# Kernel tuning notes

Hardware: AMD Instinct MI355X
Metric: run time of the kernel (lower is better)

Reference implementation:

```python
import jax, jax.numpy as jnp
import numpy as np

N, E, G = 50000, 800000, 128          # nodes, edges, graphs
L, T, F = 4, 4, 20                    # conv layers, towers, per-tower width
D = T * F                             # 80 = hidden dim
EDGE_DIM = 16
AVG_DEG_LOG = float(np.log(17.0))     # avg_deg['log'] for avg in-degree ~16
EPS_STD = 1e-5
EPS_BN = 1e-5


def setup_inputs() -> dict:
    ks = iter(jax.random.split(jax.random.key(0), 32))
    rn = lambda *s: jax.random.normal(next(ks), s, jnp.float32) * 0.1
    return dict(
        x=jax.random.randint(next(ks), (N, 9), 0, 16),
        edge_index=jax.random.randint(next(ks), (2, E), 0, N),
        batch=jnp.sort(jax.random.randint(next(ks), (N,), 0, G)),
        edge_attr=rn(E, EDGE_DIM),
        atom_emb=rn(9, 16, D),
        edge_w=rn(L, EDGE_DIM, F), edge_b=jnp.zeros((L, F), jnp.float32),
        pre_w1=rn(L, T, 3 * F, F), pre_b1=jnp.zeros((L, T, F), jnp.float32),
        pre_w2=rn(L, T, F, F), pre_b2=jnp.zeros((L, T, F), jnp.float32),
        post_w1=rn(L, T, 13 * F, F), post_b1=jnp.zeros((L, T, F), jnp.float32),
        post_w2=rn(L, T, F, F), post_b2=jnp.zeros((L, T, F), jnp.float32),
        lin_w=rn(L, D, D), lin_b=jnp.zeros((L, D), jnp.float32),
        bn_g=jnp.ones((L, D), jnp.float32), bn_b=jnp.zeros((L, D), jnp.float32),
        mlp_w1=rn(D, 40), mlp_b1=jnp.zeros(40, jnp.float32),
        mlp_w2=rn(40, 20), mlp_b2=jnp.zeros(20, jnp.float32),
        mlp_w3=rn(20, 1), mlp_b3=jnp.zeros(1, jnp.float32),
    )


def _net(x, edge_index, batch, edge_attr, atom_emb, edge_w, edge_b, pre_w1,
         pre_b1, pre_w2, pre_b2, post_w1, post_b1, post_w2, post_b2, lin_w,
         lin_b, bn_g, bn_b, mlp_w1, mlp_b1, mlp_w2, mlp_b2, mlp_w3, mlp_b3):
    src, dst = edge_index[0], edge_index[1]
    # AtomEncoder: sum of 9 categorical embeddings -> [N, D]
    h = atom_emb[jnp.arange(9)[None, :], x].sum(1)
    deg_raw = jax.ops.segment_sum(jnp.ones((E,), jnp.float32), dst, N)
    deg = jnp.clip(deg_raw, 1.0)
    has_edge = (deg_raw > 0)[:, None, None]
    d3 = deg[:, None, None]
    logd = jnp.log(deg + 1.0)[:, None, None]
    for l in range(L):  # 4 PNAConv + BN + ReLU + residual (dropout off / eval)
        xt = h.reshape(N, T, F)
        ea = edge_attr @ edge_w[l] + edge_b[l]                      # [E, F]
        # message: concat(x_i, x_j, edge) -> per-tower pre MLP
        m = jnp.concatenate([xt[dst], xt[src],
                             jnp.broadcast_to(ea[:, None, :], (E, T, F))], -1)
        m = jax.nn.relu(jnp.einsum('eti,tio->eto', m, pre_w1[l]) + pre_b1[l])
        m = jnp.einsum('eti,tio->eto', m, pre_w2[l]) + pre_b2[l]    # [E,T,F]
        # multi-aggregator scatter-reduce
        mean = jax.ops.segment_sum(m, dst, N) / d3
        msq = jax.ops.segment_sum(m * m, dst, N) / d3
        std = jnp.sqrt(jax.nn.relu(msq - mean * mean) + EPS_STD)
        mn = jnp.where(has_edge, jax.ops.segment_min(m, dst, N), 0.0)
        mx = jnp.where(has_edge, jax.ops.segment_max(m, dst, N), 0.0)
        agg = jnp.concatenate([mean, mn, mx, std], -1)              # [N,T,4F]
        # degree scalers: identity, amplification, attenuation
        out = jnp.concatenate([agg, agg * (logd / AVG_DEG_LOG),
                               agg * (AVG_DEG_LOG / logd)], -1)     # [N,T,12F]
        out = jnp.concatenate([xt, out], -1)                        # [N,T,13F]
        out = jax.nn.relu(jnp.einsum('nti,tio->nto', out, post_w1[l]) + post_b1[l])
        out = jnp.einsum('nti,tio->nto', out, post_w2[l]) + post_b2[l]
        out = out.reshape(N, D) @ lin_w[l] + lin_b[l]
        # BatchNorm over nodes (batch statistics)
        mu = out.mean(0)
        var = jnp.mean((out - mu) ** 2, axis=0)
        out = (out - mu) * (bn_g[l] / jnp.sqrt(var + EPS_BN)) + bn_b[l]
        h = jax.nn.relu(out) + h
    # global mean pool over graphs + readout MLP
    cnt = jnp.clip(jax.ops.segment_sum(jnp.ones((N,), jnp.float32), batch, G), 1.0)
    g = jax.ops.segment_sum(h, batch, G) / cnt[:, None]
    g = jax.nn.relu(g @ mlp_w1 + mlp_b1)
    g = jax.nn.relu(g @ mlp_w2 + mlp_b2)
    return g @ mlp_w3 + mlp_b3                                      # [G, 1]


def reference(x, edge_index, batch, edge_attr, atom_emb, edge_w, edge_b, pre_w1,
              pre_b1, pre_w2, pre_b2, post_w1, post_b1, post_w2, post_b2, lin_w,
              lin_b, bn_g, bn_b, mlp_w1, mlp_b1, mlp_w2, mlp_b2, mlp_w3, mlp_b3):
    return _net(x, edge_index, batch, edge_attr, atom_emb, edge_w, edge_b, pre_w1,
                pre_b1, pre_w2, pre_b2, post_w1, post_b1, post_w2, post_b2,
                lin_w, lin_b, bn_g, bn_b, mlp_w1, mlp_b1, mlp_w2, mlp_b2,
                mlp_w3, mlp_b3)
```

## Files before the change

### kernel.cpp

```cpp
#include <hip/hip_runtime.h>
#include <hip/hip_bf16.h>

#define NN 50000
#define EE 800000
#define GG 128
#define LL 4
#define TT 4
#define FF 20
#define DD 80
#define SCAN_B ((NN + 1023) / 1024)
#define TILE_N 16
#define ITEMS (TILE_N * 10)
static constexpr float AVG_LOG = 2.8332133440562162f;

typedef __fp16 half2v __attribute__((ext_vector_type(2)));

__device__ __forceinline__ float bf2f(unsigned short u) {
  return __uint_as_float((unsigned)u << 16);
}
__device__ __forceinline__ unsigned short f2bf(float f) {
  __hip_bfloat16 b = __float2bfloat16(f);
  return *(unsigned short*)&b;
}
__device__ __forceinline__ half2v pkrtz(float a, float b) {
#if __has_builtin(__builtin_amdgcn_cvt_pkrtz)
  return __builtin_amdgcn_cvt_pkrtz(a, b);
#else
  half2v h; h.x = (__fp16)a; h.y = (__fp16)b; return h;
#endif
}
__device__ __forceinline__ float fdot2(half2v a, half2v b, float c) {
#if __has_builtin(__builtin_amdgcn_fdot2)
  return __builtin_amdgcn_fdot2(a, b, c, false);
#else
  return fmaf((float)a.x, (float)b.x, fmaf((float)a.y, (float)b.y, c));
#endif
}
__device__ __forceinline__ half2v u2h2(unsigned int u) {
  return __builtin_bit_cast(half2v, u);
}
__device__ __forceinline__ unsigned int h22u(half2v h) {
  return __builtin_bit_cast(unsigned int, h);
}
__device__ __forceinline__ unsigned int packh2_rne(float a, float b) {
  half2v h; h.x = (__fp16)a; h.y = (__fp16)b;
  return h22u(h);
}
__device__ __forceinline__ unsigned int pack_bf16(float a, float b) {
  return (unsigned int)f2bf(a) | ((unsigned int)f2bf(b) << 16);
}

__global__ __launch_bounds__(256) void k_h(const int* __restrict__ x,
                                           const float* __restrict__ atom_emb,
                                           float* __restrict__ h) {
  int idx = blockIdx.x * 256 + threadIdx.x;
  if (idx >= NN * DD) return;
  int n = idx / DD, d = idx - n * DD;
  const int* xr = x + n * 9;
  float acc = 0.f;
#pragma unroll
  for (int i = 0; i < 9; ++i) {
    int v = xr[i];
    acc += atom_emb[(i * 16 + v) * DD + d];
  }
  h[idx] = acc;
}

__global__ __launch_bounds__(256) void k_deg(const int* __restrict__ ei, int* __restrict__ cnt) {
  int e = blockIdx.x * 256 + threadIdx.x;
  if (e >= EE) return;
  atomicAdd(&cnt[ei[EE + e]], 1);
}

__global__ __launch_bounds__(1024) void k_scan_sum(const int* __restrict__ cnt, int* __restrict__ bsum) {
  __shared__ int red[1024];
  int tid = threadIdx.x;
  int i = blockIdx.x * 1024 + tid;
  red[tid] = (i < NN) ? cnt[i] : 0;
  __syncthreads();
  for (int off = 512; off > 0; off >>= 1) {
    if (tid < off) red[tid] += red[tid + off];
    __syncthreads();
  }
  if (tid == 0) bsum[blockIdx.x] = red[0];
}

__global__ void k_scan_top(const int* __restrict__ bsum, int* __restrict__ boff,
                           int* __restrict__ row_ptr) {
  if (threadIdx.x == 0 && blockIdx.x == 0) {
    int acc = 0;
    for (int b = 0; b < SCAN_B; ++b) { boff[b] = acc; acc += bsum[b]; }
    row_ptr[NN] = acc;
  }
}

__global__ __launch_bounds__(1024) void k_scan_apply(const int* __restrict__ cnt,
                                                     const int* __restrict__ boff,
                                                     int* __restrict__ row_ptr,
                                                     int* __restrict__ cursor) {
  __shared__ int sm[1024];
  int tid = threadIdx.x;
  int i = blockIdx.x * 1024 + tid;
  int v = (i < NN) ? cnt[i] : 0;
  sm[tid] = v;
  __syncthreads();
  for (int off = 1; off < 1024; off <<= 1) {
    int t = (tid >= off) ? sm[tid - off] : 0;
    __syncthreads();
    sm[tid] += t;
    __syncthreads();
  }
  int excl = boff[blockIdx.x] + sm[tid] - v;
  if (i < NN) { row_ptr[i] = excl; cursor[i] = excl; }
}

__global__ __launch_bounds__(256) void k_csrfill(const int* __restrict__ ei,
                                                 int* __restrict__ cursor,
                                                 int* __restrict__ csr_src,
                                                 int* __restrict__ csr_eid,
                                                 int* __restrict__ csr_dst) {
  int e = blockIdx.x * 256 + threadIdx.x;
  if (e >= EE) return;
  int dst = ei[EE + e];
  int slot = atomicAdd(&cursor[dst], 1);
  csr_src[slot] = ei[e];
  csr_eid[slot] = e;
  csr_dst[slot] = dst;
}

__global__ __launch_bounds__(256) void k_eagather(const int* __restrict__ csr_eid,
                                                  const float* __restrict__ edge_attr,
                                                  unsigned int* __restrict__ ea16) {
  int sl = blockIdx.x * 256 + threadIdx.x;
  if (sl >= EE) return;
  int e = csr_eid[sl];
  const float4* ap = (const float4*)(edge_attr + (size_t)e * 16);
  uint4 o0, o1;
  float4 v0 = ap[0], v1 = ap[1], v2 = ap[2], v3 = ap[3];
  o0.x = packh2_rne(v0.x, v0.y); o0.y = packh2_rne(v0.z, v0.w);
  o0.z = packh2_rne(v1.x, v1.y); o0.w = packh2_rne(v1.z, v1.w);
  o1.x = packh2_rne(v2.x, v2.y); o1.y = packh2_rne(v2.z, v2.w);
  o1.z = packh2_rne(v3.x, v3.y); o1.w = packh2_rne(v3.z, v3.w);
  uint4* op = (uint4*)(ea16 + (size_t)sl * 8);
  op[0] = o0; op[1] = o1;
}

__global__ __launch_bounds__(256) void k_nodeparams(const int* __restrict__ cnt,
                                                    float* __restrict__ inv_deg,
                                                    float* __restrict__ s1a,
                                                    float* __restrict__ s2a) {
  int n = blockIdx.x * 256 + threadIdx.x;
  if (n >= NN) return;
  int c = cnt[n];
  float deg = (c > 0) ? (float)c : 1.0f;
  inv_deg[n] = 1.0f / deg;
  float logd = logf(deg + 1.0f);
  s1a[n] = logd / AVG_LOG;
  s2a[n] = AVG_LOG / logd;
}

__global__ __launch_bounds__(64) void k_wcomb(const float* __restrict__ edge_w,
                                              const float* __restrict__ edge_b,
                                              const float* __restrict__ pre_w1,
                                              const float* __restrict__ pre_b1,
                                              const float* __restrict__ pre_w2,
                                              const float* __restrict__ post_w1,
                                              const float* __restrict__ post_w2,
                                              unsigned int* __restrict__ wcpk,
                                              unsigned int* __restrict__ w2pk,
                                              unsigned int* __restrict__ q1pk,
                                              unsigned int* __restrict__ q2pk,
                                              float* __restrict__ biasc,
                                              float* __restrict__ colsum, int l) {
  int t = blockIdx.x;
  int wt = l * TT + t;
  int j = threadIdx.x;
  if (t == 0) {
    for (int i = threadIdx.x; i < 2 * DD; i += 64) colsum[i] = 0.f;
  }
  if (j >= FF) return;
  const float* W1 = pre_w1 + (size_t)wt * 1200;
  const float* W2 = pre_w2 + (size_t)wt * 400;
  const float* ew = edge_w + (size_t)l * 16 * FF;
  const float* eb = edge_b + (size_t)l * FF;
  float col[16];
  for (int i = 0; i < 16; ++i) {
    float acc = 0.f;
#pragma unroll
    for (int f = 0; f < FF; ++f) acc = fmaf(ew[i * FF + f], W1[(40 + f) * FF + j], acc);
    col[i] = acc;
  }
#pragma unroll
  for (int i2 = 0; i2 < 8; ++i2)
    wcpk[((size_t)t * FF + j) * 8 + i2] = packh2_rne(col[2 * i2], col[2 * i2 + 1]);
#pragma unroll
  for (int i2 = 0; i2 < 10; ++i2)
    w2pk[((size_t)t * FF + j) * 10 + i2] = packh2_rne(W2[(2 * i2) * FF + j], W2[(2 * i2 + 1) * FF + j]);
  float b = pre_b1[wt * FF + j];
#pragma unroll
  for (int f = 0; f < FF; ++f) b = fmaf(eb[f], W1[(40 + f) * FF + j], b);
  biasc[t * FF + j] = b;
  const float* Q1 = post_w1 + (size_t)wt * 5200;
  const float* Q2 = post_w2 + (size_t)wt * 400;
  for (int i2 = 0; i2 < 120; ++i2) {
    int blk = i2 / 40, k = i2 - blk * 40;
    int r0 = 20 + 80 * blk + 2 * k;
    q1pk[((size_t)t * 120 + i2) * FF + j] = packh2_rne(Q1[r0 * FF + j], Q1[(r0 + 1) * FF + j]);
  }
#pragma unroll
  for (int i2 = 0; i2 < 10; ++i2)
    q2pk[((size_t)t * 10 + i2) * FF + j] = packh2_rne(Q2[(2 * i2) * FF + j], Q2[(2 * i2 + 1) * FF + j]);
}

__global__ __launch_bounds__(256) void k_prenode(
    const float* __restrict__ h, const float* __restrict__ pre_w1,
    const float* __restrict__ biasc,
    unsigned short* __restrict__ predD, unsigned short* __restrict__ predS, int l) {
  int tid = threadIdx.x;
  int t = tid >> 6, lane = tid & 63;
  int n = blockIdx.x * 64 + lane;
  if (n >= NN) return;
  int wt_u = __builtin_amdgcn_readfirstlane(l * TT + t);
  const float* W1 = pre_w1 + (size_t)wt_u * 1200;
  const float* bc = biasc + t * FF;
  float xt[FF];
  {
    const float4* pp = (const float4*)(h + (size_t)n * DD + t * FF);
#pragma unroll
    for (int i = 0; i < 5; ++i) { float4 v = pp[i]; xt[i*4]=v.x; xt[i*4+1]=v.y; xt[i*4+2]=v.z; xt[i*4+3]=v.w; }
  }
  float d[FF], s[FF];
#pragma unroll
  for (int j = 0; j < FF; ++j) { d[j] = bc[j]; s[j] = 0.f; }
#pragma unroll
  for (int i = 0; i < FF; ++i) {
    float a = xt[i];
#pragma unroll
    for (int j = 0; j < FF; ++j) {
      d[j] = fmaf(a, W1[i * FF + j], d[j]);
      s[j] = fmaf(a, W1[(FF + i) * FF + j], s[j]);
    }
  }
  ushort4* pd = (ushort4*)(predD + (size_t)n * DD + t * FF);
  ushort4* ps = (ushort4*)(predS + (size_t)n * DD + t * FF);
#pragma unroll
  for (int i = 0; i < 5; ++i) {
    pd[i] = make_ushort4(f2bf(d[i*4]), f2bf(d[i*4+1]), f2bf(d[i*4+2]), f2bf(d[i*4+3]));
    ps[i] = make_ushort4(f2bf(s[i*4]), f2bf(s[i*4+1]), f2bf(s[i*4+2]), f2bf(s[i*4+3]));
  }
}

__global__ __launch_bounds__(256, 4) void k_preagg(
    const unsigned short* __restrict__ predD,
    const unsigned short* __restrict__ predS,
    const unsigned int* __restrict__ ea16,
    const int* __restrict__ csr_src,
    const int* __restrict__ csr_dst,
    const int* __restrict__ row_ptr,
    const float* __restrict__ inv_deg,
    const unsigned int* __restrict__ wcpk,
    const unsigned int* __restrict__ w2pk,
    const float* __restrict__ pre_b2,
    unsigned short* __restrict__ aggbuf,
    int l) {
  __shared__ int nbr[TILE_N + 1];
  __shared__ float dDs[TT][TILE_N * FF];
  __shared__ unsigned int m2w[TT][128 * 11];
  int tid = threadIdx.x;
  int t = tid >> 6, lane = tid & 63;
  int t_u = __builtin_amdgcn_readfirstlane(t);
  int n0 = blockIdx.x * TILE_N;
  const unsigned int* Wcp = wcpk + (size_t)t_u * FF * 8;
  const unsigned int* W2p = w2pk + (size_t)t_u * FF * 10;
  const float* b2 = pre_b2 + (size_t)(l * TT + t_u) * FF;

  if (tid <= TILE_N) {
    int node = n0 + tid; if (node > NN) node = NN;
    nbr[tid] = row_ptr[node];
  }
  for (int i = lane; i < TILE_N * FF; i += 64) {
    int ni = i / FF, ch = i - ni * FF;
    int node = n0 + ni;
    dDs[t][i] = (node < NN) ? bf2f(predD[(size_t)node * DD + t_u * FF + ch]) : 0.f;
  }
  __syncthreads();
  int tbeg = nbr[0], tend = nbr[TILE_N];

  int itN[3], itP[3], itB[3], itE[3];
#pragma unroll
  for (int k = 0; k < 3; ++k) {
    int it = lane + 64 * k;
    bool v = it < ITEMS;
    int nd = v ? (it / 10) : 0;
    itN[k] = nd;
    itP[k] = v ? (it - nd * 10) : 0;
    itB[k] = v ? nbr[nd] : 0;
    itE[k] = v ? nbr[nd + 1] : 0;
  }
  float sS[3][2], sQ[3][2], sN[3][2], sX[3][2];
#pragma unroll
  for (int k = 0; k < 3; ++k) {
    sS[k][0] = 0.f; sS[k][1] = 0.f; sQ[k][0] = 0.f; sQ[k][1] = 0.f;
    sN[k][0] = 3.4e38f; sN[k][1] = 3.4e38f; sX[k][0] = -3.4e38f; sX[k][1] = -3.4e38f;
  }

  for (int wb = tbeg; wb < tend; wb += 128) {
#pragma unroll
    for (int e = 0; e < 2; ++e) {
      int sl = lane + 64 * e;
      int p = wb + sl;
      if (p < tend) {
        int src = csr_src[p];
        int ni = csr_dst[p] - n0;
        float m1[FF];
        {
          const float4* dd = (const float4*)(&dDs[t][ni * FF]);
          const ushort4* qq = (const ushort4*)(predS + (size_t)src * DD + t_u * FF);
#pragma unroll
          for (int i = 0; i < 5; ++i) {
            float4 d4 = dd[i];
            ushort4 v = qq[i];
            m1[i*4+0] = d4.x + bf2f(v.x);
            m1[i*4+1] = d4.y + bf2f(v.y);
            m1[i*4+2] = d4.z + bf2f(v.z);
            m1[i*4+3] = d4.w + bf2f(v.w);
          }
        }
        half2v eap[8];
        {
          const uint4* ep = (const uint4*)(ea16 + (size_t)p * 8);
          uint4 e0 = ep[0], e1 = ep[1];
          eap[0] = u2h2(e0.x); eap[1] = u2h2(e0.y); eap[2] = u2h2(e0.z); eap[3] = u2h2(e0.w);
          eap[4] = u2h2(e1.x); eap[5] = u2h2(e1.y); eap[6] = u2h2(e1.z); eap[7] = u2h2(e1.w);
        }
#pragma unroll
        for (int j = 0; j < FF; ++j) {
          float c = m1[j];
#pragma unroll
          for (int i2 = 0; i2 < 8; ++i2) c = fdot2(eap[i2], u2h2(Wcp[j * 8 + i2]), c);
          m1[j] = c;
        }
        half2v mp[10];
#pragma unroll
        for (int pr = 0; pr < 10; ++pr)
          mp[pr] = pkrtz(fmaxf(m1[2*pr], 0.f), fmaxf(m1[2*pr+1], 0.f));
        float m2[FF];
#pragma unroll
        for (int j = 0; j < FF; ++j) {
          float c = b2[j];
#pragma unroll
          for (int i2 = 0; i2 < 10; ++i2) c = fdot2(mp[i2], u2h2(W2p[j * 10 + i2]), c);
          m2[j] = c;
        }
        unsigned int* row = &m2w[t][sl * 11];
#pragma unroll
        for (int pr = 0; pr < 10; ++pr) row[pr] = h22u(pkrtz(m2[2*pr], m2[2*pr+1]));
      }
    }
    __syncthreads();
    int we = (wb + 128 < tend) ? (wb + 128) : tend;
#pragma unroll
    for (int k = 0; k < 3; ++k) {
      int lo = itB[k] > wb ? itB[k] : wb;
      int hi = itE[k] < we ? itE[k] : we;
      for (int s = lo; s < hi; ++s) {
        half2v h2 = u2h2(m2w[t][(s - wb) * 11 + itP[k]]);
        float v0 = (float)h2.x, v1 = (float)h2.y;
        sS[k][0] += v0; sQ[k][0] = fmaf(v0, v0, sQ[k][0]);
        sN[k][0] = fminf(sN[k][0], v0); sX[k][0] = fmaxf(sX[k][0], v0);
        sS[k][1] += v1; sQ[k][1] = fmaf(v1, v1, sQ[k][1]);
        sN[k][1] = fminf(sN[k][1], v1); sX[k][1] = fmaxf(sX[k][1], v1);
      }
    }
    __syncthreads();
  }

#pragma unroll
  for (int k = 0; k < 3; ++k) {
    int it = lane + 64 * k;
    if (it < ITEMS) {
      int n = n0 + itN[k];
      if (n < NN) {
        float inv = inv_deg[n];
        bool noe = (itE[k] <= itB[k]);
        float mu0 = sS[k][0] * inv, mu1 = sS[k][1] * inv;
        float sd0 = sqrtf(fmaxf(sQ[k][0] * inv - mu0 * mu0, 0.f) + 1e-5f);
        float sd1 = sqrtf(fmaxf(sQ[k][1] * inv - mu1 * mu1, 0.f) + 1e-5f);
        float mn0 = noe ? 0.f : sN[k][0], mn1 = noe ? 0.f : sN[k][1];
        float mx0 = noe ? 0.f : sX[k][0], mx1 = noe ? 0.f : sX[k][1];
        unsigned short* ab = aggbuf + ((size_t)n * 4 + t_u) * 80;
        ((unsigned int*)(ab))[itP[k]]      = pack_bf16(mu0, mu1);
        ((unsigned int*)(ab + 20))[itP[k]] = pack_bf16(mn0, mn1);
        ((unsigned int*)(ab + 40))[itP[k]] = pack_bf16(mx0, mx1);
        ((unsigned int*)(ab + 60))[itP[k]] = pack_bf16(sd0, sd1);
      }
    }
  }
}

__global__ __launch_bounds__(256) void k_postlin(
    const float* __restrict__ h, const unsigned short* __restrict__ aggbuf,
    const float* __restrict__ s1a, const float* __restrict__ s2a,
    const float* __restrict__ post_w1, const float* __restrict__ post_b1,
    const unsigned int* __restrict__ q1pk, const unsigned int* __restrict__ q2pk,
    const float* __restrict__ post_b2,
    const float* __restrict__ lin_w, const float* __restrict__ lin_b,
    float* __restrict__ outl, float* __restrict__ colsum, int l) {
  __shared__ float rows[5280];
  __shared__ unsigned int lq1[TT * 120 * FF];
  __shared__ unsigned int lq2[TT * 10 * FF];
  int tid = threadIdx.x;
  int t = tid >> 6, lane = tid & 63;
  int t_u = __builtin_amdgcn_readfirstlane(t);
  int wt_u = __builtin_amdgcn_readfirstlane(l * TT + t);
  int n = blockIdx.x * 64 + lane;
  bool nvalid = (n < NN);

  float xt[FF];
  uint4 araw[10];
  {
    const float4* pp = (const float4*)(h + (size_t)(nvalid ? n : 0) * DD + t_u * FF);
#pragma unroll
    for (int i = 0; i < 5; ++i) { float4 v = pp[i]; xt[i*4]=v.x; xt[i*4+1]=v.y; xt[i*4+2]=v.z; xt[i*4+3]=v.w; }
    const uint4* ap = (const uint4*)(aggbuf + ((size_t)(nvalid ? n : 0) * 4 + t_u) * 80);
#pragma unroll
    for (int q = 0; q < 10; ++q) araw[q] = ap[q];
  }
  float c1 = s1a[nvalid ? n : 0], c2 = s2a[nvalid ? n : 0];

  {
    const uint4* s1p = (const uint4*)q1pk;
    uint4* d1 = (uint4*)lq1;
    for (int i = tid; i < TT * 120 * FF / 4; i += 256) d1[i] = s1p[i];
    const uint4* s2p = (const uint4*)q2pk;
    uint4* d2 = (uint4*)lq2;
    for (int i = tid; i < TT * 10 * FF / 4; i += 256) d2[i] = s2p[i];
  }
  __syncthreads();

  const float* Q1 = post_w1 + (size_t)wt_u * 5200;
  const float* B1 = post_b1 + (size_t)wt_u * FF;
  const float* B2 = post_b2 + (size_t)wt_u * FF;
  const unsigned int* q1 = lq1 + t_u * 120 * FF;
  const unsigned int* q2 = lq2 + t_u * 10 * FF;
  if (nvalid) {
    half2v c1p = pkrtz(c1, c1), c2p = pkrtz(c2, c2);
    half2v a0p[40];
#pragma unroll
    for (int q = 0; q < 10; ++q) {
      unsigned int w[4] = {araw[q].x, araw[q].y, araw[q].z, araw[q].w};
#pragma unroll
      for (int k = 0; k < 4; ++k) {
        unsigned int u = w[k];
        float lo = __uint_as_float(u << 16);
        float hi = __uint_as_float(u & 0xffff0000u);
        a0p[q * 4 + k] = pkrtz(lo, hi);
      }
    }
    float o1[FF];
#pragma unroll
    for (int j = 0; j < FF; ++j) o1[j] = B1[j];
#pragma unroll
    for (int i = 0; i < FF; ++i) {
      float a = xt[i];
#pragma unroll
      for (int j = 0; j < FF; ++j) o1[j] = fmaf(a, Q1[i * FF + j], o1[j]);
    }
#pragma unroll 2
    for (int k = 0; k < 40; ++k) {
      half2v act = a0p[k];
      const unsigned int* wr = q1 + k * FF;
#pragma unroll
      for (int j = 0; j < FF; ++j) o1[j] = fdot2(act, u2h2(wr[j]), o1[j]);
    }
#pragma unroll 2
    for (int k = 0; k < 40; ++k) {
      half2v act = a0p[k] * c1p;
      const unsigned int* wr = q1 + (40 + k) * FF;
#pragma unroll
      for (int j = 0; j < FF; ++j) o1[j] = fdot2(act, u2h2(wr[j]), o1[j]);
    }
#pragma unroll 2
    for (int k = 0; k < 40; ++k) {
      half2v act = a0p[k] * c2p;
      const unsigned int* wr = q1 + (80 + k) * FF;
#pragma unroll
      for (int j = 0; j < FF; ++j) o1[j] = fdot2(act, u2h2(wr[j]), o1[j]);
    }
    half2v o1p[10];
#pragma unroll
    for (int i2 = 0; i2 < 10; ++i2)
      o1p[i2] = pkrtz(fmaxf(o1[2*i2], 0.f), fmaxf(o1[2*i2+1], 0.f));
    float o2[FF];
#pragma unroll
    for (int j = 0; j < FF; ++j) o2[j] = B2[j];
#pragma unroll 2
    for (int i2 = 0; i2 < 10; ++i2) {
      half2v act = o1p[i2];
      const unsigned int* wr = q2 + i2 * FF;
#pragma unroll
      for (int j = 0; j < FF; ++j) o2[j] = fdot2(act, u2h2(wr[j]), o2[j]);
    }
#pragma unroll
    for (int j = 0; j < FF; ++j) rows[lane * 81 + t_u * FF + j] = o2[j];
  } else {
#pragma unroll
    for (int j = 0; j < FF; ++j) rows[lane * 81 + t_u * FF + j] = 0.f;
  }
  __syncthreads();

  int n2 = blockIdx.x * 64 + lane;
  const float* WlG = lin_w + (size_t)l * DD * DD + t_u * FF;
  float acc[FF];
#pragma unroll
  for (int j = 0; j < FF; ++j) acc[j] = lin_b[l * DD + t_u * FF + j];
  for (int i = 0; i < DD; ++i) {
    float r = rows[lane * 81 + i];
    const float* wl = WlG + i * DD;
#pragma unroll
    for (int j = 0; j < FF; ++j) acc[j] = fmaf(r, wl[j], acc[j]);
  }
  bool valid = (n2 < NN);
  __syncthreads();

#pragma unroll
  for (int j = 0; j < FF; ++j) rows[(t_u * FF + j) * 66 + lane] = valid ? acc[j] : 0.f;
  __syncthreads();
  if (tid < DD) {
    float s = 0.f;
    for (int k = 0; k < 64; ++k) s += rows[tid * 66 + k];
    atomicAdd(&colsum[tid], s);
  }
  {
    int nb = blockIdx.x * 64;
    for (int i = tid; i < 64 * 20; i += 256) {
      int nl = i / 20;
      int c4 = (i - nl * 20) * 4;
      int gn = nb + nl;
      if (gn < NN) {
        float4 v = make_float4(rows[(c4 + 0) * 66 + nl], rows[(c4 + 1) * 66 + nl],
                               rows[(c4 + 2) * 66 + nl], rows[(c4 + 3) * 66 + nl]);
        *(float4*)(outl + (size_t)gn * DD + c4) = v;
      }
    }
  }
  __syncthreads();
#pragma unroll
  for (int j = 0; j < FF; ++j) rows[(t_u * FF + j) * 66 + lane] = valid ? acc[j] * acc[j] : 0.f;
  __syncthreads();
  if (tid < DD) {
    float s = 0.f;
    for (int k = 0; k < 64; ++k) s += rows[tid * 66 + k];
    atomicAdd(&colsum[DD + tid], s);
  }
}

__global__ __launch_bounds__(256) void k_bnapply(const float* __restrict__ outl,
                                                 const float* __restrict__ colsum,
                                                 const float* __restrict__ bn_g,
                                                 const float* __restrict__ bn_b,
                                                 float* __restrict__ h, int l) {
  __shared__ float sc[DD], ofs[DD];
  int tid = threadIdx.x;
  if (tid < DD) {
    float mu = colsum[tid] * (1.0f / NN);
    float var = colsum[DD + tid] * (1.0f / NN) - mu * mu;
    float s = bn_g[l * DD + tid] * rsqrtf(var + 1e-5f);
    sc[tid] = s;
    ofs[tid] = bn_b[l * DD + tid] - mu * s;
  }
  __syncthreads();
  int idx = blockIdx.x * 256 + tid;
  if (idx >= NN * DD) return;
  int d = idx % DD;
  float v = fmaf(outl[idx], sc[d], ofs[d]);
  h[idx] += fmaxf(v, 0.f);
}

__global__ __launch_bounds__(256) void k_gcnt(const int* __restrict__ batch, int* __restrict__ gcnt) {
  __shared__ int hcnt[GG];
  int tid = threadIdx.x;
  if (tid < GG) hcnt[tid] = 0;
  __syncthreads();
  int n = blockIdx.x * 256 + tid;
  if (n < NN) atomicAdd(&hcnt[batch[n]], 1);
  __syncthreads();
  if (tid < GG && hcnt[tid] > 0) atomicAdd(&gcnt[tid], hcnt[tid]);
}

__global__ void k_gstart(const int* __restrict__ gcnt, int* __restrict__ gstart) {
  if (threadIdx.x == 0 && blockIdx.x == 0) {
    int acc = 0;
    for (int g = 0; g < GG; ++g) { gstart[g] = acc; acc += gcnt[g]; }
  }
}

__global__ __launch_bounds__(320) void k_gmean(const float* __restrict__ h,
                                               const int* __restrict__ gstart,
                                               const int* __restrict__ gcnt,
                                               float* __restrict__ gbuf) {
  __shared__ float red[320];
  int g = blockIdx.x, tid = threadIdx.x;
  int nl = tid / DD, d = tid - nl * DD;
  int start = gstart[g], c = gcnt[g];
  float acc = 0.f;
  for (int r = start + nl; r < start + c; r += 4) acc += h[(size_t)r * DD + d];
  red[tid] = acc;
  __syncthreads();
  if (tid < DD) {
    float s = red[tid] + red[tid + DD] + red[tid + 2 * DD] + red[tid + 3 * DD];
    float cf = (c > 0) ? (float)c : 1.0f;
    gbuf[g * DD + tid] = s / cf;
  }
}

__global__ __launch_bounds__(64) void k_mlp(const float* __restrict__ gbuf,
                                            const float* __restrict__ w1, const float* __restrict__ b1,
                                            const float* __restrict__ w2, const float* __restrict__ b2,
                                            const float* __restrict__ w3, const float* __restrict__ b3,
                                            float* __restrict__ out) {
  __shared__ float row[DD];
  __shared__ float t1[40];
  __shared__ float t2[20];
  int g = blockIdx.x, tid = threadIdx.x;
  for (int i = tid; i < DD; i += 64) row[i] = gbuf[g * DD + i];
  __syncthreads();
  if (tid < 40) {
    float acc = b1[tid];
#pragma unroll
    for (int i = 0; i < DD; ++i) acc = fmaf(row[i], w1[i * 40 + tid], acc);
    t1[tid] = fmaxf(acc, 0.f);
  }
  __syncthreads();
  if (tid < 20) {
    float acc = b2[tid];
#pragma unroll
    for (int i = 0; i < 40; ++i) acc = fmaf(t1[i], w2[i * 20 + tid], acc);
    t2[tid] = fmaxf(acc, 0.f);
  }
  __syncthreads();
  if (tid == 0) {
    float acc = b3[0];
#pragma unroll
    for (int i = 0; i < 20; ++i) acc = fmaf(t2[i], w3[i], acc);
    out[g] = acc;
  }
}

extern "C" void kernel_launch(void* const* d_in, const int* in_sizes, int n_in,
                              void* d_out, int out_size, void* d_ws, size_t ws_size,
                              hipStream_t stream) {
  const int*   x         = (const int*)d_in[0];
  const int*   ei        = (const int*)d_in[1];
  const int*   batch     = (const int*)d_in[2];
  const float* edge_attr = (const float*)d_in[3];
  const float* atom_emb  = (const float*)d_in[4];
  const float* edge_w    = (const float*)d_in[5];
  const float* edge_b    = (const float*)d_in[6];
  const float* pre_w1    = (const float*)d_in[7];
  const float* pre_b1    = (const float*)d_in[8];
  const float* pre_w2    = (const float*)d_in[9];
  const float* pre_b2    = (const float*)d_in[10];
  const float* post_w1   = (const float*)d_in[11];
  const float* post_b1   = (const float*)d_in[12];
  const float* post_w2   = (const float*)d_in[13];
  const float* post_b2   = (const float*)d_in[14];
  const float* lin_w     = (const float*)d_in[15];
  const float* lin_b     = (const float*)d_in[16];
  const float* bn_g      = (const float*)d_in[17];
  const float* bn_b      = (const float*)d_in[18];
  const float* mlp_w1    = (const float*)d_in[19];
  const float* mlp_b1    = (const float*)d_in[20];
  const float* mlp_w2    = (const float*)d_in[21];
  const float* mlp_b2    = (const float*)d_in[22];
  const float* mlp_w3    = (const float*)d_in[23];
  const float* mlp_b3    = (const float*)d_in[24];
  float* out = (float*)d_out;

  char* ws = (char*)d_ws;
  size_t off = 0;
  auto alloc = [&](size_t bytes) -> void* {
    void* p = ws + off;
    off += (bytes + 15) & ~(size_t)15;
    return p;
  };
  float* h       = (float*)alloc((size_t)NN * DD * 4);
  float* outl    = (float*)alloc((size_t)NN * DD * 4);
  unsigned short* predD = (unsigned short*)alloc((size_t)NN * DD * 2);
  unsigned short* predS = (unsigned short*)alloc((size_t)NN * DD * 2);
  int*   csr_src = (int*)alloc((size_t)EE * 4);
  int*   csr_eid = (int*)alloc((size_t)EE * 4);
  int*   csr_dst = (int*)alloc((size_t)EE * 4);
  unsigned int* ea16 = (unsigned int*)alloc((size_t)EE * 8 * 4);
  int*   row_ptr = (int*)alloc((size_t)(NN + 1) * 4);
  int*   cnt     = (int*)alloc((size_t)NN * 4);
  int*   cursor  = (int*)alloc((size_t)NN * 4);
  float* inv_deg = (float*)alloc((size_t)NN * 4);
  float* s1a     = (float*)alloc((size_t)NN * 4);
  float* s2a     = (float*)alloc((size_t)NN * 4);
  float* colsum  = (float*)alloc(2 * DD * 4);
  float* gbuf    = (float*)alloc((size_t)GG * DD * 4);
  unsigned int* wcpk  = (unsigned int*)alloc((size_t)TT * FF * 8 * 4);
  unsigned int* w2pk  = (unsigned int*)alloc((size_t)TT * FF * 10 * 4);
  unsigned int* q1pk  = (unsigned int*)alloc((size_t)TT * 120 * FF * 4);
  unsigned int* q2pk  = (unsigned int*)alloc((size_t)TT * 10 * FF * 4);
  float* biasc   = (float*)alloc((size_t)TT * FF * 4);
  int*   bsum    = (int*)alloc((size_t)SCAN_B * 4);
  int*   boff    = (int*)alloc((size_t)SCAN_B * 4);
  int*   gcnt    = (int*)alloc((size_t)GG * 4);
  int*   gstart  = (int*)alloc((size_t)(GG + 1) * 4);
  unsigned short* aggbuf = (unsigned short*)alloc((size_t)NN * 4 * 80 * 2);
  (void)in_sizes; (void)n_in; (void)out_size; (void)ws_size;

  hipMemsetAsync(cnt, 0, (size_t)NN * 4, stream);
  k_h<<<(NN * DD + 255) / 256, 256, 0, stream>>>(x, atom_emb, h);
  k_deg<<<(EE + 255) / 256, 256, 0, stream>>>(ei, cnt);
  k_scan_sum<<<SCAN_B, 1024, 0, stream>>>(cnt, bsum);
  k_scan_top<<<1, 64, 0, stream>>>(bsum, boff, row_ptr);
  k_scan_apply<<<SCAN_B, 1024, 0, stream>>>(cnt, boff, row_ptr, cursor);
  k_csrfill<<<(EE + 255) / 256, 256, 0, stream>>>(ei, cursor, csr_src, csr_eid, csr_dst);
  k_eagather<<<(EE + 255) / 256, 256, 0, stream>>>(csr_eid, edge_attr, ea16);
  k_nodeparams<<<(NN + 255) / 256, 256, 0, stream>>>(cnt, inv_deg, s1a, s2a);

  int tilesA = (NN + TILE_N - 1) / TILE_N;
  int blocksPL = (NN + 63) / 64;
  for (int l = 0; l < LL; ++l) {
    k_wcomb<<<TT, 64, 0, stream>>>(edge_w, edge_b, pre_w1, pre_b1, pre_w2,
        post_w1, post_w2, wcpk, w2pk, q1pk, q2pk, biasc, colsum, l);
    k_prenode<<<(NN + 63) / 64, 256, 0, stream>>>(h, pre_w1, biasc, predD, predS, l);
    k_preagg<<<tilesA, 256, 0, stream>>>(predD, predS, ea16, csr_src, csr_dst, row_ptr,
        inv_deg, wcpk, w2pk, pre_b2, aggbuf, l);
    k_postlin<<<blocksPL, 256, 0, stream>>>(h, aggbuf, s1a, s2a,
        post_w1, post_b1, q1pk, q2pk, post_b2, lin_w, lin_b, outl, colsum, l);
    k_bnapply<<<(NN * DD + 255) / 256, 256, 0, stream>>>(outl, colsum, bn_g, bn_b, h, l);
  }

  hipMemsetAsync(gcnt, 0, (size_t)GG * 4, stream);
  k_gcnt<<<(NN + 255) / 256, 256, 0, stream>>>(batch, gcnt);
  k_gstart<<<1, 64, 0, stream>>>(gcnt, gstart);
  k_gmean<<<GG, 320, 0, stream>>>(h, gstart, gcnt, gbuf);
  k_mlp<<<GG, 64, 0, stream>>>(gbuf, mlp_w1, mlp_b1, mlp_w2, mlp_b2, mlp_w3, mlp_b3, out);
}
```

Baseline: 1.358 ms.

## Fuse BatchNorm apply into next layer's pre-node kernel and shrink postlin LDS

For layers after the first, the BatchNorm, ReLU and residual update is folded into a new k_bnpre kernel. It recomputes h from outl and the previous layer's column sums, writes h back and immediately computes the pre-node projections. This removes one full read-write pass over h per layer and one launch. The column-sum buffers are double-buffered so that zeroing in k_wcomb does not clobber the statistics still needed. Separately, k_postlin now stages its intermediate rows as packed fp16 in a shared union buffer to reduce LDS use, at some precision cost.

```diff
diff --git a/kernel.cpp b/kernel.cpp
--- a/kernel.cpp
+++ b/kernel.cpp
@@ -171,12 +171,12 @@
                                               unsigned int* __restrict__ q1pk,
                                               unsigned int* __restrict__ q2pk,
                                               float* __restrict__ biasc,
-                                              float* __restrict__ colsum, int l) {
+                                              float* __restrict__ colsum_cur, int l) {
   int t = blockIdx.x;
   int wt = l * TT + t;
   int j = threadIdx.x;
   if (t == 0) {
-    for (int i = threadIdx.x; i < 2 * DD; i += 64) colsum[i] = 0.f;
+    for (int i = threadIdx.x; i < 2 * DD; i += 64) colsum_cur[i] = 0.f;
   }
   if (j >= FF) return;
   const float* W1 = pre_w1 + (size_t)wt * 1200;
@@ -243,6 +243,72 @@
   }
   ushort4* pd = (ushort4*)(predD + (size_t)n * DD + t * FF);
   ushort4* ps = (ushort4*)(predS + (size_t)n * DD + t * FF);
+#pragma unroll
+  for (int i = 0; i < 5; ++i) {
+    pd[i] = make_ushort4(f2bf(d[i*4]), f2bf(d[i*4+1]), f2bf(d[i*4+2]), f2bf(d[i*4+3]));
+    ps[i] = make_ushort4(f2bf(s[i*4]), f2bf(s[i*4+1]), f2bf(s[i*4+2]), f2bf(s[i*4+3]));
+  }
+}
+
+__global__ __launch_bounds__(256) void k_bnpre(
+    const float* __restrict__ outl, const float* __restrict__ colsum_prev,
+    const float* __restrict__ bn_g, const float* __restrict__ bn_b,
+    float* __restrict__ h,
+    const float* __restrict__ pre_w1, const float* __restrict__ biasc,
+    unsigned short* __restrict__ predD, unsigned short* __restrict__ predS,
+    int lprev, int l) {
+  __shared__ float sc[DD], ofs[DD];
+  int tid = threadIdx.x;
+  int t = tid >> 6, lane = tid & 63;
+  if (tid < DD) {
+    float mu = colsum_prev[tid] * (1.0f / NN);
+    float var = colsum_prev[DD + tid] * (1.0f / NN) - mu * mu;
+    float s = bn_g[lprev * DD + tid] * rsqrtf(var + 1e-5f);
+    sc[tid] = s;
+    ofs[tid] = bn_b[lprev * DD + tid] - mu * s;
+  }
+  __syncthreads();
+  int n = blockIdx.x * 64 + lane;
+  if (n >= NN) return;
+  int wt_u = __builtin_amdgcn_readfirstlane(l * TT + t);
+  int t_u = __builtin_amdgcn_readfirstlane(t);
+  const float* W1 = pre_w1 + (size_t)wt_u * 1200;
+  const float* bc = biasc + t_u * FF;
+  float xt[FF];
+  {
+    const float4* po = (const float4*)(outl + (size_t)n * DD + t_u * FF);
+    const float4* ph = (const float4*)(h + (size_t)n * DD + t_u * FF);
+#pragma unroll
+    for (int i = 0; i < 5; ++i) {
+      float4 vo = po[i];
+      float4 vh = ph[i];
+      int d0 = t_u * FF + i * 4;
+      xt[i*4+0] = vh.x + fmaxf(fmaf(vo.x, sc[d0+0], ofs[d0+0]), 0.f);
+      xt[i*4+1] = vh.y + fmaxf(fmaf(vo.y, sc[d0+1], ofs[d0+1]), 0.f);
+      xt[i*4+2] = vh.z + fmaxf(fmaf(vo.z, sc[d0+2], ofs[d0+2]), 0.f);
+      xt[i*4+3] = vh.w + fmaxf(fmaf(vo.w, sc[d0+3], ofs[d0+3]), 0.f);
+    }
+  }
+  {
+    float4* ph = (float4*)(h + (size_t)n * DD + t_u * FF);
+#pragma unroll
+    for (int i = 0; i < 5; ++i)
+      ph[i] = make_float4(xt[i*4], xt[i*4+1], xt[i*4+2], xt[i*4+3]);
+  }
+  float d[FF], s[FF];
+#pragma unroll
+  for (int j = 0; j < FF; ++j) { d[j] = bc[j]; s[j] = 0.f; }
+#pragma unroll
+  for (int i = 0; i < FF; ++i) {
+    float a = xt[i];
+#pragma unroll
+    for (int j = 0; j < FF; ++j) {
+      d[j] = fmaf(a, W1[i * FF + j], d[j]);
+      s[j] = fmaf(a, W1[(FF + i) * FF + j], s[j]);
+    }
+  }
+  ushort4* pd = (ushort4*)(predD + (size_t)n * DD + t_u * FF);
+  ushort4* ps = (ushort4*)(predS + (size_t)n * DD + t_u * FF);
 #pragma unroll
   for (int i = 0; i < 5; ++i) {
     pd[i] = make_ushort4(f2bf(d[i*4]), f2bf(d[i*4+1]), f2bf(d[i*4+2]), f2bf(d[i*4+3]));
@@ -406,9 +472,11 @@
     const float* __restrict__ post_b2,
     const float* __restrict__ lin_w, const float* __restrict__ lin_b,
     float* __restrict__ outl, float* __restrict__ colsum, int l) {
-  __shared__ float rows[5280];
-  __shared__ unsigned int lq1[TT * 120 * FF];
-  __shared__ unsigned int lq2[TT * 10 * FF];
+  __shared__ unsigned int smem[13024];
+  unsigned int* rowsU = smem;
+  unsigned int* lq1 = smem + 2624;
+  unsigned int* lq2 = smem + 2624 + 9600;
+  float* tbuf = (float*)(smem + 2624);
   int tid = threadIdx.x;
   int t = tid >> 6, lane = tid & 63;
   int t_u = __builtin_amdgcn_readfirstlane(t);
@@ -502,10 +570,11 @@
       for (int j = 0; j < FF; ++j) o2[j] = fdot2(act, u2h2(wr[j]), o2[j]);
     }
 #pragma unroll
-    for (int j = 0; j < FF; ++j) rows[lane * 81 + t_u * FF + j] = o2[j];
+    for (int pr = 0; pr < 10; ++pr)
+      rowsU[lane * 41 + t_u * 10 + pr] = packh2_rne(o2[2*pr], o2[2*pr+1]);
   } else {
 #pragma unroll
-    for (int j = 0; j < FF; ++j) rows[lane * 81 + t_u * FF + j] = 0.f;
+    for (int pr = 0; pr < 10; ++pr) rowsU[lane * 41 + t_u * 10 + pr] = 0;
   }
   __syncthreads();
 
@@ -514,21 +583,26 @@
   float acc[FF];
 #pragma unroll
   for (int j = 0; j < FF; ++j) acc[j] = lin_b[l * DD + t_u * FF + j];
-  for (int i = 0; i < DD; ++i) {
-    float r = rows[lane * 81 + i];
-    const float* wl = WlG + i * DD;
-#pragma unroll
-    for (int j = 0; j < FF; ++j) acc[j] = fmaf(r, wl[j], acc[j]);
+  for (int i2 = 0; i2 < 40; ++i2) {
+    half2v rp = u2h2(rowsU[lane * 41 + i2]);
+    float r0 = (float)rp.x, r1 = (float)rp.y;
+    const float* wl0 = WlG + (2 * i2) * DD;
+    const float* wl1 = WlG + (2 * i2 + 1) * DD;
+#pragma unroll
+    for (int j = 0; j < FF; ++j) {
+      acc[j] = fmaf(r0, wl0[j], acc[j]);
+      acc[j] = fmaf(r1, wl1[j], acc[j]);
+    }
   }
   bool valid = (n2 < NN);
   __syncthreads();
 
 #pragma unroll
-  for (int j = 0; j < FF; ++j) rows[(t_u * FF + j) * 66 + lane] = valid ? acc[j] : 0.f;
+  for (int j = 0; j < FF; ++j) tbuf[(t_u * FF + j) * 66 + lane] = valid ? acc[j] : 0.f;
   __syncthreads();
   if (tid < DD) {
     float s = 0.f;
-    for (int k = 0; k < 64; ++k) s += rows[tid * 66 + k];
+    for (int k = 0; k < 64; ++k) s += tbuf[tid * 66 + k];
     atomicAdd(&colsum[tid], s);
   }
   {
@@ -538,19 +612,19 @@
       int c4 = (i - nl * 20) * 4;
       int gn = nb + nl;
       if (gn < NN) {
-        float4 v = make_float4(rows[(c4 + 0) * 66 + nl], rows[(c4 + 1) * 66 + nl],
-                               rows[(c4 + 2) * 66 + nl], rows[(c4 + 3) * 66 + nl]);
+        float4 v = make_float4(tbuf[(c4 + 0) * 66 + nl], tbuf[(c4 + 1) * 66 + nl],
+                               tbuf[(c4 + 2) * 66 + nl], tbuf[(c4 + 3) * 66 + nl]);
         *(float4*)(outl + (size_t)gn * DD + c4) = v;
       }
     }
   }
   __syncthreads();
 #pragma unroll
-  for (int j = 0; j < FF; ++j) rows[(t_u * FF + j) * 66 + lane] = valid ? acc[j] * acc[j] : 0.f;
+  for (int j = 0; j < FF; ++j) tbuf[(t_u * FF + j) * 66 + lane] = valid ? acc[j] * acc[j] : 0.f;
   __syncthreads();
   if (tid < DD) {
     float s = 0.f;
-    for (int k = 0; k < 64; ++k) s += rows[tid * 66 + k];
+    for (int k = 0; k < 64; ++k) s += tbuf[tid * 66 + k];
     atomicAdd(&colsum[DD + tid], s);
   }
 }
@@ -698,7 +772,8 @@
   float* inv_deg = (float*)alloc((size_t)NN * 4);
   float* s1a     = (float*)alloc((size_t)NN * 4);
   float* s2a     = (float*)alloc((size_t)NN * 4);
-  float* colsum  = (float*)alloc(2 * DD * 4);
+  float* colsumA = (float*)alloc(2 * DD * 4);
+  float* colsumB = (float*)alloc(2 * DD * 4);
   float* gbuf    = (float*)alloc((size_t)GG * DD * 4);
   unsigned int* wcpk  = (unsigned int*)alloc((size_t)TT * FF * 8 * 4);
   unsigned int* w2pk  = (unsigned int*)alloc((size_t)TT * FF * 10 * 4);
@@ -712,6 +787,8 @@
   unsigned short* aggbuf = (unsigned short*)alloc((size_t)NN * 4 * 80 * 2);
   (void)in_sizes; (void)n_in; (void)out_size; (void)ws_size;
 
+  float* cs[2] = {colsumA, colsumB};
+
   hipMemsetAsync(cnt, 0, (size_t)NN * 4, stream);
   k_h<<<(NN * DD + 255) / 256, 256, 0, stream>>>(x, atom_emb, h);
   k_deg<<<(EE + 255) / 256, 256, 0, stream>>>(ei, cnt);
@@ -726,14 +803,19 @@
   int blocksPL = (NN + 63) / 64;
   for (int l = 0; l < LL; ++l) {
     k_wcomb<<<TT, 64, 0, stream>>>(edge_w, edge_b, pre_w1, pre_b1, pre_w2,
-        post_w1, post_w2, wcpk, w2pk, q1pk, q2pk, biasc, colsum, l);
-    k_prenode<<<(NN + 63) / 64, 256, 0, stream>>>(h, pre_w1, biasc, predD, predS, l);
+        post_w1, post_w2, wcpk, w2pk, q1pk, q2pk, biasc, cs[l & 1], l);
+    if (l == 0) {
+      k_prenode<<<blocksPL, 256, 0, stream>>>(h, pre_w1, biasc, predD, predS, l);
+    } else {
+      k_bnpre<<<blocksPL, 256, 0, stream>>>(outl, cs[(l - 1) & 1], bn_g, bn_b, h,
+          pre_w1, biasc, predD, predS, l - 1, l);
+    }
     k_preagg<<<tilesA, 256, 0, stream>>>(predD, predS, ea16, csr_src, csr_dst, row_ptr,
         inv_deg, wcpk, w2pk, pre_b2, aggbuf, l);
     k_postlin<<<blocksPL, 256, 0, stream>>>(h, aggbuf, s1a, s2a,
-        post_w1, post_b1, q1pk, q2pk, post_b2, lin_w, lin_b, outl, colsum, l);
-    k_bnapply<<<(NN * DD + 255) / 256, 256, 0, stream>>>(outl, colsum, bn_g, bn_b, h, l);
-  }
+        post_w1, post_b1, q1pk, q2pk, post_b2, lin_w, lin_b, outl, cs[l & 1], l);
+  }
+  k_bnapply<<<(NN * DD + 255) / 256, 256, 0, stream>>>(outl, cs[(LL - 1) & 1], bn_g, bn_b, h, LL - 1);
 
   hipMemsetAsync(gcnt, 0, (size_t)GG * 4, stream);
   k_gcnt<<<(NN + 255) / 256, 256, 0, stream>>>(batch, gcnt);
```

Measured after the change: 1.359 ms. Within noise of the previous version (+0.1%).
